# Kernel tuning notes

Measured on AMD Instinct MI355X. Metric: run time of the kernel, lower is better.

## Reference

```python
import jax, jax.numpy as jnp
import numpy as np

N, D, A, K, E = 8192, 256, 1024, 65, 4096

def setup_inputs() -> dict:
    key = jax.random.key(0)
    ks = jax.random.split(key, 8)
    s = 0.02  # linear-init scale to keep activations sane
    return {
        "embedding": jax.random.normal(ks[0], (N, D), jnp.float32),
        "data": jax.random.randint(ks[1], (E, 2), 0, N, jnp.int64),
        "Wq": jax.random.normal(ks[2], (D, A), jnp.float32) * s,
        "bq": jnp.zeros((A,), jnp.float32),
        "Wk": jax.random.normal(ks[3], (D, A), jnp.float32) * s,
        "bk": jnp.zeros((A,), jnp.float32),
        "Wv": jax.random.normal(ks[4], (D, A), jnp.float32) * s,
        "bv": jnp.zeros((A,), jnp.float32),
        "W_edge": jax.random.normal(ks[5], (K, A, A), jnp.float32) * s,
    }

def reference(embedding, data, Wq, bq, Wk, bk, Wv, bv, W_edge):
    # NodeSelfAttention: dense full attention over all N nodes
    Q = embedding @ Wq + bq            # [N, A]
    Km = embedding @ Wk + bk           # [N, A]
    V = embedding @ Wv + bv            # [N, A]
    scale = 1.0 / jnp.sqrt(jnp.float32(D))  # note: sqrt(num_feats)=sqrt(256), as in source
    scores = (Q @ Km.T) * scale        # [N, N]
    attn = jax.nn.softmax(scores, axis=-1)
    attn_emb = attn @ V                # [N, A]
    # gather edge endpoints
    h_u = attn_emb[data[:, 0]]         # [E, A]
    h_v = attn_emb[data[:, 1]]         # [E, A]
    # KWayPred: out[e,k] = h_u[e] @ W_edge[k] @ h_v[e]
    # (source computes full ExE matmul per k and takes diag; this is the
    #  equivalent O(E*K*A^2) bilinear-diag form)
    t = jnp.einsum('ed,kdf->ekf', h_u, W_edge)   # [E, K, A]
    out = jnp.einsum('ekf,ef->ek', t, h_v)       # [E, K]
    return out
```

## Files before the change

### kernel.cpp

```cpp
#include <hip/hip_runtime.h>
#include <cstdio>
#include <cstdint>

#define NTOK 8192
#define DIM  256
#define AA   1024
#define KE   65
#define EE   4096

typedef unsigned short u16;
typedef __attribute__((ext_vector_type(4))) float   f32x4;
typedef __attribute__((ext_vector_type(8))) short   bf16x8;
typedef __attribute__((ext_vector_type(8))) unsigned short u16x8;

#define DEVI __device__ __forceinline__

DEVI u16 f2bf(float f) {
  union { float f; unsigned u; } x; x.f = f;
  unsigned r = x.u + 0x7FFFu + ((x.u >> 16) & 1u);
  return (u16)(r >> 16);
}
DEVI float bf2f(u16 h) {
  union { unsigned u; float f; } x; x.u = ((unsigned)h) << 16;
  return x.f;
}

DEVI void gload16(const void* g, void* l) {
  __builtin_amdgcn_global_load_lds(
      (const __attribute__((address_space(1))) void*)g,
      (__attribute__((address_space(3))) void*)l,
      16, 0, 0);
}

#define BM 128
#define BN 128
#define BK 64

template<int EPI, bool BF32>
__global__ __launch_bounds__(256)
void gemm_bt(const u16* __restrict__ A, int lda,
             const void* __restrict__ Bptr, int ldb,
             int MT, int NT, int K,
             u16* __restrict__ o_q, u16* __restrict__ o_k, u16* __restrict__ o_vt,
             const float* __restrict__ biasc,
             u16* __restrict__ o_s, float scale, int ldc,
             const u16* __restrict__ Hu, float* __restrict__ o_e)
{
  const int nb  = MT * NT;
  const int per = nb >> 3;
  int bid = blockIdx.x;
  bid = (bid & 7) * per + (bid >> 3);
  const int mt = bid % MT, nt = bid / MT;
  const int m0 = mt * BM, n0 = nt * BN;

  __shared__ u16 As[BM * BK];
  __shared__ u16 Bs[BN * BK];

  const int tid  = threadIdx.x;
  const int lane = tid & 63, wave = tid >> 6;
  const int wm = (wave >> 1) * 64, wn = (wave & 1) * 64;

  f32x4 acc[4][4];
#pragma unroll
  for (int m = 0; m < 4; ++m)
#pragma unroll
    for (int n = 0; n < 4; ++n) acc[m][n] = f32x4{0.f, 0.f, 0.f, 0.f};

  const u16*   Bh = (const u16*)Bptr;
  const float* Bf = (const float*)Bptr;

  const int KT = K / BK;
  for (int kt = 0; kt < KT; ++kt) {
    const int k0 = kt * BK;
#pragma unroll
    for (int it = 0; it < 4; ++it) {
      int o = it * 4096 + wave * 1024 + lane * 16;
      int r = o >> 7;
      int c = (o & 127) >> 1;
      gload16(A + (size_t)(m0 + r) * lda + k0 + c,
              &As[(it * 4096 + wave * 1024) >> 1]);
    }
    if constexpr (!BF32) {
#pragma unroll
      for (int it = 0; it < 4; ++it) {
        int o = it * 4096 + wave * 1024 + lane * 16;
        int r = o >> 7;
        int c = (o & 127) >> 1;
        gload16(Bh + (size_t)(n0 + r) * ldb + k0 + c,
                &Bs[(it * 4096 + wave * 1024) >> 1]);
      }
    } else {
#pragma unroll
      for (int it = 0; it < 8; ++it) {
        int e = it * 1024 + tid * 4;
        int r = e >> 6, c = e & 63;
        const float4 v = *(const float4*)(Bf + (size_t)(n0 + r) * ldb + k0 + c);
        ushort4 h;
        h.x = f2bf(v.x); h.y = f2bf(v.y); h.z = f2bf(v.z); h.w = f2bf(v.w);
        *(ushort4*)&Bs[r * BK + c] = h;
      }
    }
    asm volatile("s_waitcnt vmcnt(0)" ::: "memory");
    __syncthreads();

#pragma unroll
    for (int kk = 0; kk < 2; ++kk) {
      const int ro = lane & 15;
      const int ko = kk * 32 + (lane >> 4) * 8;
      bf16x8 af[4], bfg[4];
#pragma unroll
      for (int m = 0; m < 4; ++m)
        af[m] = *(const bf16x8*)&As[(wm + m * 16 + ro) * BK + ko];
#pragma unroll
      for (int n = 0; n < 4; ++n)
        bfg[n] = *(const bf16x8*)&Bs[(wn + n * 16 + ro) * BK + ko];
#pragma unroll
      for (int m = 0; m < 4; ++m)
#pragma unroll
        for (int n = 0; n < 4; ++n)
          acc[m][n] = __builtin_amdgcn_mfma_f32_16x16x32_bf16(
              af[m], bfg[n], acc[m][n], 0, 0, 0);
    }
    __syncthreads();
  }

  const int rgrp = lane >> 4, cid = lane & 15;

  if constexpr (EPI == 0) {
#pragma unroll
    for (int m = 0; m < 4; ++m)
#pragma unroll
      for (int n = 0; n < 4; ++n)
#pragma unroll
        for (int j = 0; j < 4; ++j) {
          int row = m0 + wm + m * 16 + rgrp * 4 + j;
          int col = n0 + wn + n * 16 + cid;
          float v = acc[m][n][j] + biasc[col];
          u16 h = f2bf(v);
          if (col < 1024)       o_q[(size_t)row * AA + col] = h;
          else if (col < 2048)  o_k[(size_t)row * AA + (col - 1024)] = h;
          else                  o_vt[(size_t)(col - 2048) * NTOK + row] = h;
        }
  } else if constexpr (EPI == 1) {
#pragma unroll
    for (int m = 0; m < 4; ++m)
#pragma unroll
      for (int n = 0; n < 4; ++n)
#pragma unroll
        for (int j = 0; j < 4; ++j) {
          int row = m0 + wm + m * 16 + rgrp * 4 + j;
          int col = n0 + wn + n * 16 + cid;
          o_s[(size_t)row * ldc + col] = f2bf(acc[m][n][j] * scale);
        }
  } else {
    const int kidx  = n0 >> 10;
    const int dbase = (n0 & 1023) + wn;
#pragma unroll
    for (int m = 0; m < 4; ++m)
#pragma unroll
      for (int j = 0; j < 4; ++j) {
        int row = m0 + wm + m * 16 + rgrp * 4 + j;
        float p = 0.f;
#pragma unroll
        for (int n = 0; n < 4; ++n) {
          int d = dbase + n * 16 + cid;
          p += acc[m][n][j] * bf2f(Hu[(size_t)row * AA + d]);
        }
        p += __shfl_xor(p, 1, 64);
        p += __shfl_xor(p, 2, 64);
        p += __shfl_xor(p, 4, 64);
        p += __shfl_xor(p, 8, 64);
        if (cid == 0) atomicAdd(&o_e[(size_t)row * KE + kidx], p);
      }
  }
}

__global__ __launch_bounds__(256)
void softmax_rows(u16* __restrict__ S)
{
  const size_t base = (size_t)blockIdx.x * 8192;
  const int tid = threadIdx.x;
  const int lane = tid & 63, wave = tid >> 6;
  float v[32];
#pragma unroll
  for (int c = 0; c < 4; ++c) {
    u16x8 u = *(const u16x8*)&S[base + c * 2048 + tid * 8];
#pragma unroll
    for (int j = 0; j < 8; ++j) v[c * 8 + j] = bf2f(u[j]);
  }
  float mx = -1e30f;
#pragma unroll
  for (int i = 0; i < 32; ++i) mx = fmaxf(mx, v[i]);
#pragma unroll
  for (int off = 1; off < 64; off <<= 1) mx = fmaxf(mx, __shfl_xor(mx, off, 64));
  __shared__ float r1[4], r2[4];
  if (lane == 0) r1[wave] = mx;
  __syncthreads();
  mx = fmaxf(fmaxf(r1[0], r1[1]), fmaxf(r1[2], r1[3]));

  float s = 0.f;
#pragma unroll
  for (int i = 0; i < 32; ++i) { v[i] = __expf(v[i] - mx); s += v[i]; }
#pragma unroll
  for (int off = 1; off < 64; off <<= 1) s += __shfl_xor(s, off, 64);
  if (lane == 0) r2[wave] = s;
  __syncthreads();
  s = r2[0] + r2[1] + r2[2] + r2[3];
  const float inv = 1.f / s;
#pragma unroll
  for (int c = 0; c < 4; ++c) {
    u16x8 u;
#pragma unroll
    for (int j = 0; j < 8; ++j) u[j] = f2bf(v[c * 8 + j] * inv);
    *(u16x8*)&S[base + c * 2048 + tid * 8] = u;
  }
}

__global__ __launch_bounds__(256)
void gather_rows(const unsigned* __restrict__ dw, const u16* __restrict__ AE,
                 u16* __restrict__ Hu, u16* __restrict__ Hv)
{
  bool i64 = true;
#pragma unroll
  for (int w = 1; w < 32; w += 2) i64 = i64 && (dw[w] == 0u);
  const int e = blockIdx.x;
  const unsigned iu = i64 ? dw[4 * e]     : dw[2 * e];
  const unsigned iv = i64 ? dw[4 * e + 2] : dw[2 * e + 1];
  const int t = threadIdx.x;
  *(ushort4*)&Hu[(size_t)e * AA + t * 4] = *(const ushort4*)&AE[(size_t)iu * AA + t * 4];
  *(ushort4*)&Hv[(size_t)e * AA + t * 4] = *(const ushort4*)&AE[(size_t)iv * AA + t * 4];
}

__global__ __launch_bounds__(256)
void init_misc(float* __restrict__ out_e, const float* __restrict__ bq,
               const float* __restrict__ bk, const float* __restrict__ bv,
               float* __restrict__ biasc)
{
  const int i = blockIdx.x * 256 + threadIdx.x;
  if (i < EE * KE) out_e[i] = 0.f;
  if (i < 1024) {
    biasc[i]        = bq[i];
    biasc[1024 + i] = bk[i];
    biasc[2048 + i] = bv[i];
  }
}

__global__ __launch_bounds__(256)
void cvt_f32_bf16_v4(const float* __restrict__ src, u16* __restrict__ dst, int n4)
{
  for (int i = blockIdx.x * 256 + threadIdx.x; i < n4; i += gridDim.x * 256) {
    float4 v = ((const float4*)src)[i];
    ushort4 h; h.x = f2bf(v.x); h.y = f2bf(v.y); h.z = f2bf(v.z); h.w = f2bf(v.w);
    ((ushort4*)dst)[i] = h;
  }
}

__global__ __launch_bounds__(256)
void build_wT(const float* __restrict__ Wq, const float* __restrict__ Wk,
              const float* __restrict__ Wv, u16* __restrict__ WT)
{
  const int nn = blockIdx.x;
  const int d  = threadIdx.x;
  const float* W = (nn < 1024) ? Wq : ((nn < 2048) ? Wk : Wv);
  WT[nn * DIM + d] = f2bf(W[(size_t)d * AA + (nn & 1023)]);
}

extern "C" void kernel_launch(void* const* d_in, const int* in_sizes, int n_in,
                              void* d_out, int out_size, void* d_ws, size_t ws_size,
                              hipStream_t stream)
{
  (void)in_sizes; (void)out_size;
  if (n_in < 9) return;
  const float*    emb  = (const float*)d_in[0];
  const unsigned* data = (const unsigned*)d_in[1];
  const float* Wq = (const float*)d_in[2];
  const float* bq = (const float*)d_in[3];
  const float* Wk = (const float*)d_in[4];
  const float* bk = (const float*)d_in[5];
  const float* Wv = (const float*)d_in[6];
  const float* bv = (const float*)d_in[7];
  const float* We = (const float*)d_in[8];
  float* out = (float*)d_out;

  char* ws = (char*)d_ws;
  size_t off = 0;
  auto alloc = [&](size_t bytes) -> void* {
    void* p = ws + off;
    off += (bytes + 255) & ~(size_t)255;
    return p;
  };
  u16*   emb_b = (u16*)alloc((size_t)NTOK * DIM * 2);
  u16*   WT    = (u16*)alloc((size_t)3072 * DIM * 2);
  float* biasc = (float*)alloc(3072 * 4);
  u16*   Qb    = (u16*)alloc((size_t)NTOK * AA * 2);
  u16*   Kb    = (u16*)alloc((size_t)NTOK * AA * 2);
  u16*   Vt    = (u16*)alloc((size_t)AA * NTOK * 2);
  u16*   AE    = (u16*)alloc((size_t)NTOK * AA * 2);
  u16*   Hu    = (u16*)alloc((size_t)EE * AA * 2);
  u16*   Hv    = (u16*)alloc((size_t)EE * AA * 2);

  const size_t webf_bytes = ((size_t)KE * AA * AA * 2 + 255) & ~(size_t)255;
  u16* We_b = nullptr;
  if (off + webf_bytes + (size_t)1024 * NTOK * 2 <= ws_size) {
    We_b = (u16*)(ws + off);
    off += webf_bytes;
  }

  int chunk = NTOK;
  while (chunk > 128 && off + (size_t)chunk * NTOK * 2 > ws_size) chunk >>= 1;
  u16* Sc = (u16*)alloc((size_t)chunk * NTOK * 2);
  if (off > ws_size) {
    fprintf(stderr, "kernel_launch: ws too small (need %zu, have %zu)\n", off, ws_size);
    return;
  }

  init_misc<<<(EE * KE) / 256, 256, 0, stream>>>(out, bq, bk, bv, biasc);
  cvt_f32_bf16_v4<<<2048, 256, 0, stream>>>(emb, emb_b, NTOK * DIM / 4);
  build_wT<<<3072, 256, 0, stream>>>(Wq, Wk, Wv, WT);
  if (We_b)
    cvt_f32_bf16_v4<<<4096, 256, 0, stream>>>(We, We_b, KE * AA * AA / 4);

  gemm_bt<0, false><<<64 * 24, 256, 0, stream>>>(
      emb_b, DIM, WT, DIM, 64, 24, DIM,
      Qb, Kb, Vt, biasc, nullptr, 0.f, 0, nullptr, nullptr);

  const int nch = NTOK / chunk;
  for (int ci = 0; ci < nch; ++ci) {
    const u16* Qc = Qb + (size_t)ci * chunk * AA;
    gemm_bt<1, false><<<(chunk / 128) * 64, 256, 0, stream>>>(
        Qc, AA, Kb, AA, chunk / 128, 64, AA,
        nullptr, nullptr, nullptr, nullptr, Sc, 0.0625f, NTOK, nullptr, nullptr);
    softmax_rows<<<chunk, 256, 0, stream>>>(Sc);
    gemm_bt<1, false><<<(chunk / 128) * 8, 256, 0, stream>>>(
        Sc, NTOK, Vt, NTOK, chunk / 128, 8, NTOK,
        nullptr, nullptr, nullptr, nullptr,
        AE + (size_t)ci * chunk * AA, 1.0f, AA, nullptr, nullptr);
  }

  gather_rows<<<EE, 256, 0, stream>>>(data, AE, Hu, Hv);

  if (We_b)
    gemm_bt<3, false><<<32 * 520, 256, 0, stream>>>(
        Hv, AA, We_b, AA, 32, 520, AA,
        nullptr, nullptr, nullptr, nullptr, nullptr, 0.f, 0, Hu, out);
  else
    gemm_bt<3, true><<<32 * 520, 256, 0, stream>>>(
        Hv, AA, We, AA, 32, 520, AA,
        nullptr, nullptr, nullptr, nullptr, nullptr, 0.f, 0, Hu, out);
}
```

Baseline: 1.759 ms.

## Add 256x256 eight-wave bf16 GEMM with interleaved staging for QK and edge GEMMs

```diff
diff --git a/kernel.cpp b/kernel.cpp
--- a/kernel.cpp
+++ b/kernel.cpp
@@ -30,6 +30,176 @@
       (const __attribute__((address_space(1))) void*)g,
       (__attribute__((address_space(3))) void*)l,
       16, 0, 0);
+}
+
+DEVI void barx() {
+  asm volatile("" ::: "memory");
+  __builtin_amdgcn_s_barrier();
+  asm volatile("" ::: "memory");
+}
+
+DEVI void stage_half(const u16* __restrict__ g0, int ld, char* dst, int tid) {
+#pragma unroll
+  for (int rr = 0; rr < 2; ++rr) {
+    int o = rr * 8192 + (tid >> 6) * 1024 + (tid & 63) * 16;
+    int q = o ^ (((o >> 7) & 7) << 4);
+    gload16(g0 + (size_t)(q >> 7) * ld + ((q & 127) >> 1),
+            dst + rr * 8192 + (tid >> 6) * 1024);
+  }
+}
+
+template<int EPI>
+__global__ __launch_bounds__(512, 2)
+void gemm8(const u16* __restrict__ A, int lda,
+           const u16* __restrict__ B, int ldb,
+           int MT, int NT, int K,
+           u16* __restrict__ o_s, float scale, int ldc,
+           const u16* __restrict__ Hu, float* __restrict__ o_e)
+{
+  __shared__ __align__(16) char lds[131072];
+  char* ldsA = lds;
+  char* ldsB = lds + 65536;
+
+  const int nb = MT * NT, per = nb >> 3;
+  int bid = blockIdx.x;
+  bid = (bid & 7) * per + (bid >> 3);
+  const int mt = bid % MT, nt = bid / MT;
+  const int m0 = mt * 256, n0 = nt * 256;
+
+  const int tid = threadIdx.x, lane = tid & 63, wave = tid >> 6;
+  const int wm = (wave >> 2) * 128;
+  const int wn = (wave & 3) * 64;
+  const int wnl = (wave & 1) * 64;
+  const int KT = K >> 6;
+
+#define STAGE_A(tk, h) stage_half(A + (size_t)(m0 + (h)*128) * lda + (size_t)(tk)*64, lda, \
+                                  ldsA + ((tk)&1) * 32768 + (h) * 16384, tid)
+#define STAGE_B(tk, h) stage_half(B + (size_t)(n0 + (h)*128) * ldb + (size_t)(tk)*64, ldb, \
+                                  ldsB + ((tk)&1) * 32768 + (h) * 16384, tid)
+
+  f32x4 acc[8][4];
+#pragma unroll
+  for (int m = 0; m < 8; ++m)
+#pragma unroll
+    for (int n = 0; n < 4; ++n) acc[m][n] = f32x4{0.f, 0.f, 0.f, 0.f};
+
+  STAGE_A(0, 0); STAGE_A(0, 1); STAGE_B(0, 0); STAGE_B(0, 1);
+  STAGE_A(1, 0); STAGE_A(1, 1); STAGE_B(1, 0);
+  asm volatile("s_waitcnt vmcnt(6)" ::: "memory");
+  barx();
+
+  const int r15 = lane & 15, g16 = (lane >> 4) << 4;
+
+  for (int t = 0; t < KT; ++t) {
+    const char* Abh = ldsA + (t & 1) * 32768 + (wm >> 7) * 16384;
+    const char* Bbh = ldsB + (t & 1) * 32768 + (wn >> 7) * 16384;
+
+    bf16x8 a[8][2], b[4][2];
+#pragma unroll
+    for (int m = 0; m < 8; ++m)
+#pragma unroll
+      for (int kk = 0; kk < 2; ++kk) {
+        int p = (m * 16 + r15) * 128 + kk * 64 + g16;
+        p ^= ((p >> 7) & 7) << 4;
+        a[m][kk] = *(const bf16x8*)(Abh + p);
+      }
+#pragma unroll
+    for (int n = 0; n < 4; ++n)
+#pragma unroll
+      for (int kk = 0; kk < 2; ++kk) {
+        int p = (wnl + n * 16 + r15) * 128 + kk * 64 + g16;
+        p ^= ((p >> 7) & 7) << 4;
+        b[n][kk] = *(const bf16x8*)(Bbh + p);
+      }
+    if (t + 1 < KT) STAGE_B(t + 1, 1);
+    asm volatile("s_waitcnt lgkmcnt(0)" ::: "memory");
+    barx();
+    __builtin_amdgcn_s_setprio(1);
+#pragma unroll
+    for (int kk = 0; kk < 2; ++kk)
+#pragma unroll
+      for (int m = 0; m < 4; ++m)
+#pragma unroll
+        for (int n = 0; n < 2; ++n)
+          acc[m][n] = __builtin_amdgcn_mfma_f32_16x16x32_bf16(a[m][kk], b[n][kk], acc[m][n], 0, 0, 0);
+    __builtin_amdgcn_s_setprio(0);
+    barx();
+
+    if (t + 2 < KT) STAGE_A(t + 2, 0);
+    barx();
+    __builtin_amdgcn_s_setprio(1);
+#pragma unroll
+    for (int kk = 0; kk < 2; ++kk)
+#pragma unroll
+      for (int m = 0; m < 4; ++m)
+#pragma unroll
+        for (int n = 2; n < 4; ++n)
+          acc[m][n] = __builtin_amdgcn_mfma_f32_16x16x32_bf16(a[m][kk], b[n][kk], acc[m][n], 0, 0, 0);
+    __builtin_amdgcn_s_setprio(0);
+    barx();
+
+    if (t + 2 < KT) STAGE_A(t + 2, 1);
+    barx();
+    __builtin_amdgcn_s_setprio(1);
+#pragma unroll
+    for (int kk = 0; kk < 2; ++kk)
+#pragma unroll
+      for (int m = 4; m < 8; ++m)
+#pragma unroll
+        for (int n = 2; n < 4; ++n)
+          acc[m][n] = __builtin_amdgcn_mfma_f32_16x16x32_bf16(a[m][kk], b[n][kk], acc[m][n], 0, 0, 0);
+    __builtin_amdgcn_s_setprio(0);
+    barx();
+
+    if (t + 2 < KT) STAGE_B(t + 2, 0);
+    barx();
+    __builtin_amdgcn_s_setprio(1);
+#pragma unroll
+    for (int kk = 0; kk < 2; ++kk)
+#pragma unroll
+      for (int m = 4; m < 8; ++m)
+#pragma unroll
+        for (int n = 0; n < 2; ++n)
+          acc[m][n] = __builtin_amdgcn_mfma_f32_16x16x32_bf16(a[m][kk], b[n][kk], acc[m][n], 0, 0, 0);
+    __builtin_amdgcn_s_setprio(0);
+    if (t + 2 < KT) asm volatile("s_waitcnt vmcnt(6)" ::: "memory");
+    else            asm volatile("s_waitcnt vmcnt(0)" ::: "memory");
+    barx();
+  }
+#undef STAGE_A
+#undef STAGE_B
+
+  const int rgrp = lane >> 4, cid = lane & 15;
+  if constexpr (EPI == 1) {
+#pragma unroll
+    for (int m = 0; m < 8; ++m)
+#pragma unroll
+      for (int n = 0; n < 4; ++n)
+#pragma unroll
+        for (int j = 0; j < 4; ++j) {
+          int row = m0 + wm + m * 16 + rgrp * 4 + j;
+          int col = n0 + wn + n * 16 + cid;
+          o_s[(size_t)row * ldc + col] = f2bf(acc[m][n][j] * scale);
+        }
+  } else {
+    const int kidx  = n0 >> 10;
+    const int dbase = (n0 & 1023) + wn;
+#pragma unroll
+    for (int m = 0; m < 8; ++m)
+#pragma unroll
+      for (int j = 0; j < 4; ++j) {
+        int row = m0 + wm + m * 16 + rgrp * 4 + j;
+        float p = 0.f;
+#pragma unroll
+        for (int n = 0; n < 4; ++n)
+          p += acc[m][n][j] * bf2f(Hu[(size_t)row * AA + dbase + n * 16 + cid]);
+        p += __shfl_xor(p, 1, 64);
+        p += __shfl_xor(p, 2, 64);
+        p += __shfl_xor(p, 4, 64);
+        p += __shfl_xor(p, 8, 64);
+        if (cid == 0) atomicAdd(&o_e[(size_t)row * KE + kidx], p);
+      }
+  }
 }
 
 #define BM 128
@@ -327,9 +497,14 @@
   const int nch = NTOK / chunk;
   for (int ci = 0; ci < nch; ++ci) {
     const u16* Qc = Qb + (size_t)ci * chunk * AA;
-    gemm_bt<1, false><<<(chunk / 128) * 64, 256, 0, stream>>>(
-        Qc, AA, Kb, AA, chunk / 128, 64, AA,
-        nullptr, nullptr, nullptr, nullptr, Sc, 0.0625f, NTOK, nullptr, nullptr);
+    if ((chunk & 255) == 0)
+      gemm8<1><<<(chunk / 256) * 32, 512, 0, stream>>>(
+          Qc, AA, Kb, AA, chunk / 256, 32, AA,
+          Sc, 0.0625f, NTOK, nullptr, nullptr);
+    else
+      gemm_bt<1, false><<<(chunk / 128) * 64, 256, 0, stream>>>(
+          Qc, AA, Kb, AA, chunk / 128, 64, AA,
+          nullptr, nullptr, nullptr, nullptr, Sc, 0.0625f, NTOK, nullptr, nullptr);
     softmax_rows<<<chunk, 256, 0, stream>>>(Sc);
     gemm_bt<1, false><<<(chunk / 128) * 8, 256, 0, stream>>>(
         Sc, NTOK, Vt, NTOK, chunk / 128, 8, NTOK,
@@ -340,9 +515,9 @@
   gather_rows<<<EE, 256, 0, stream>>>(data, AE, Hu, Hv);
 
   if (We_b)
-    gemm_bt<3, false><<<32 * 520, 256, 0, stream>>>(
-        Hv, AA, We_b, AA, 32, 520, AA,
-        nullptr, nullptr, nullptr, nullptr, nullptr, 0.f, 0, Hu, out);
+    gemm8<2><<<16 * 260, 512, 0, stream>>>(
+        Hv, AA, We_b, AA, 16, 260, AA,
+        nullptr, 0.f, 0, Hu, out);
   else
     gemm_bt<3, true><<<32 * 520, 256, 0, stream>>>(
         Hv, AA, We, AA, 32, 520, AA,
```

After: 1.965 ms. +11.7%, slower.
